# Performance work log

Measured on AMD Instinct MI355X. Metric: run time of the kernel, lower is better.

## Reference

```python
import jax, jax.numpy as jnp
import numpy as np

N = 50000      # nodes
E = 800000     # edges (avg degree 16)
H = 128        # hidden_dim
F_IN = 128     # node_in_dim
EPS = 1e-8     # torch cosine_similarity eps
ALPHA = 0.3


def _xavier(k, shape):
    fan_out, fan_in = shape
    lim = float(np.sqrt(6.0 / (fan_in + fan_out)))
    return jax.random.uniform(k, shape, minval=-lim, maxval=lim, dtype=jnp.float32)


PARAM_SHAPES = [
    ("w_lq", (H, 1)), ("w_lf", (H, F_IN)),
    ("wq0", (H, 1)), ("wq1", (H, H)), ("wq2", (H, H)),
    ("wx0", (H, F_IN)), ("wx1", (H, H)), ("wx2", (H, H)),
    ("wf0", (H, H)), ("wf1", (H, H)), ("wf2", (H, H)),
    ("m1_w1", (H, H)), ("m1_w2", (H, H)),
    ("m2_w1", (1, H)), ("m2_w2", (1, 1)),
]
BIAS_OF = {"w_lq": "b_lq", "w_lf": "b_lf", "wq0": "bq0", "wq1": "bq1", "wq2": "bq2",
           "wx0": "bx0", "wx1": "bx1", "wx2": "bx2", "wf0": "bf0", "wf1": "bf1",
           "wf2": "bf2", "m1_w1": "m1_b1", "m1_w2": "m1_b2", "m2_w1": "m2_b1", "m2_w2": "m2_b2"}


def setup_inputs() -> dict:
    key = jax.random.key(0)
    ks = jax.random.split(key, 3 + len(PARAM_SHAPES))
    inp = {
        "q": 42,
        "feats": jax.random.normal(ks[0], (N, F_IN), dtype=jnp.float32),
        "edge_index": jax.random.randint(ks[1], (2, E), 0, N, dtype=jnp.int64),
        "neg_edge_index": jax.random.randint(ks[2], (2, E), 0, N, dtype=jnp.int64),
    }
    for i, (name, shape) in enumerate(PARAM_SHAPES):
        inp[name] = _xavier(ks[3 + i], shape)
        inp[BIAS_OF[name]] = jnp.zeros((shape[0],), jnp.float32)
    return inp


def _forward(q, feats, edge_index, neg_edge_index,
             w_lq, b_lq, w_lf, b_lf,
             wq0, bq0, wq1, bq1, wq2, bq2,
             wx0, bx0, wx1, bx1, wx2, bx2,
             wf0, bf0, wf1, bf1, wf2, bf2,
             m1_w1, m1_b1, m1_w2, m1_b2,
             m2_w1, m2_b1, m2_w2, m2_b2):
    n = feats.shape[0]
    src, dst = edge_index[0], edge_index[1]

    # GCN symmetric normalization with self-loops (edge_weight = 1)
    deg = jax.ops.segment_sum(jnp.ones(src.shape[0], feats.dtype), dst, num_segments=n) + 1.0
    dis = deg ** -0.5
    norm_e = dis[src] * dis[dst]        # per-edge norm
    inv_deg = 1.0 / deg                 # self-loop norm d^-1/2 * d^-1/2

    def lin(x, W, b):
        return x @ W.T + b

    def gcn(x, W, b):
        xw = x @ W.T                                                      # [n,H]
        agg = jax.ops.segment_sum(xw[src] * norm_e[:, None], dst, num_segments=n)
        return agg + xw * inv_deg[:, None] + b

    querys = jnp.zeros((n, 1), feats.dtype).at[q, 0].set(1.0)
    querys_ = lin(querys, w_lq, b_lq)
    feats_ = lin(feats, w_lf, b_lf)

    # layer 0
    hq = jax.nn.relu(gcn(querys, wq0, bq0))
    h = jax.nn.relu(gcn(feats, wx0, bx0))
    hf = jax.nn.relu(hq + h + gcn(querys_ + feats_, wf0, bf0))
    # middle layer (num_layers - 2 == 1 iteration, eval mode: dropout identity)
    hq = jax.nn.relu(gcn(hq, wq1, bq1))
    h = jax.nn.relu(gcn(h, wx1, bx1))
    hf = jax.nn.relu(hq + h + gcn(hf, wf1, bf1))
    # final layer (no relu)
    hq = gcn(hq, wq2, bq2)
    h = gcn(h, wx2, bx2)
    hf = hq + h + gcn(hf, wf2, bf2)

    x = lin(jax.nn.relu(lin(hf, m1_w1, m1_b1)), m1_w2, m1_b2)  # mlp1

    # ---- decode (attack_type != 'proposed') ----
    q_emb = x[q]
    qn = jnp.maximum(jnp.linalg.norm(q_emb), EPS)

    def cos_q(v):  # cosine similarity of rows of v with q_emb (torch eps semantics)
        vn = jnp.maximum(jnp.linalg.norm(v, axis=-1), EPS)
        return (v @ q_emb) / (vn * qn)

    # reconstruct loss: BCE-with-logits on cosine edge scores
    pos_s = cos_q((x[src] + x[dst]) * 0.5)
    neg_s = cos_q((x[neg_edge_index[0]] + x[neg_edge_index[1]]) * 0.5)
    loss_recon = jnp.mean(jax.nn.softplus(-pos_s)) + jnp.mean(jax.nn.softplus(neg_s))

    sim_xq = cos_q(x)                                            # [n]
    sim_xx = lin(jax.nn.relu(lin(x, m2_w1, m2_b1)), m2_w2, m2_b2)[:, 0]  # mlp2
    sim = ((1.0 - ALPHA) * sim_xq + ALPHA * sim_xx) * 2.0
    return jax.nn.sigmoid(sim), loss_recon


def reference(q, feats, edge_index, neg_edge_index,
              w_lq, b_lq, w_lf, b_lf,
              wq0, bq0, wq1, bq1, wq2, bq2,
              wx0, bx0, wx1, bx1, wx2, bx2,
              wf0, bf0, wf1, bf1, wf2, bf2,
              m1_w1, m1_b1, m1_w2, m1_b2,
              m2_w1, m2_b1, m2_w2, m2_b2):
    return _forward(q, feats, edge_index, neg_edge_index,
                    w_lq, b_lq, w_lf, b_lf,
                    wq0, bq0, wq1, bq1, wq2, bq2,
                    wx0, bx0, wx1, bx1, wx2, bx2,
                    wf0, bf0, wf1, bf1, wf2, bf2,
                    m1_w1, m1_b1, m1_w2, m1_b2,
                    m2_w1, m2_b1, m2_w2, m2_b2)
```

## Files before the change

### kernel.cpp

```cpp
#include <hip/hip_runtime.h>
#include <math.h>

#define N_NODES 50000
#define N_EDGES 800000
#define EPSV 1e-8f
#define ALPHA 0.3f

typedef __attribute__((ext_vector_type(8))) unsigned short ushort8;
typedef __attribute__((ext_vector_type(4))) float floatx4;
typedef __attribute__((ext_vector_type(2))) long longx2;
typedef _Float16 half8 __attribute__((ext_vector_type(8)));
typedef _Float16 half2v __attribute__((ext_vector_type(2)));

__device__ inline unsigned short f2h(float f) {
    union { _Float16 h; unsigned short u; } c; c.h = (_Float16)f; return c.u;
}
__device__ inline float h2f(unsigned short u) {
    union { unsigned short u; _Float16 h; } c; c.u = u; return (float)c.h;
}
__device__ inline unsigned char f2e4m3(float f) {
    unsigned u = __float_as_uint(f);
    unsigned s = (u >> 24) & 0x80u;
    float af = fabsf(f);
    if (af >= 464.f) return (unsigned char)(s | 0x7Eu);
    if (af < 0.015625f) {
        int m = (int)rintf(af * 512.f);
        return (unsigned char)(s | (unsigned)m);
    }
    unsigned au = __float_as_uint(af);
    unsigned mant = au & 0x7FFFFFu;
    unsigned lsb = (mant >> 20) & 1u;
    mant += 0x7FFFFu + lsb;
    unsigned exp32 = (au >> 23) + (mant >> 23);
    mant &= 0x7FFFFFu;
    unsigned e8 = exp32 - 127u + 7u;
    return (unsigned char)(s | (e8 << 3) | (mant >> 20));
}


__global__ __launch_bounds__(256) void k_count(const int* __restrict__ ei,
                                               int* __restrict__ cnt) {
    int e = blockIdx.x * 256 + threadIdx.x;
    if (e < N_EDGES) atomicAdd(&cnt[ei[N_EDGES + e]], 1);
}

__global__ __launch_bounds__(256) void k_invdis(const int* __restrict__ cnt,
                                                float* __restrict__ dis,
                                                float* __restrict__ inv) {
    int i = blockIdx.x * 256 + threadIdx.x;
    if (i < N_NODES) {
        float d = (float)cnt[i] + 1.0f;
        dis[i] = 1.0f / sqrtf(d);
        inv[i] = 1.0f / d;
    }
}

__global__ __launch_bounds__(256) void k_scan_partial(const int* __restrict__ cnt,
                                                      int* __restrict__ partial) {
    int b = blockIdx.x, t = threadIdx.x;
    int base = b * 1024 + t * 4;
    int s = 0;
#pragma unroll
    for (int j = 0; j < 4; ++j) {
        int idx = base + j;
        if (idx < N_NODES) s += cnt[idx];
    }
#pragma unroll
    for (int m = 1; m < 64; m <<= 1) s += __shfl_xor(s, m, 64);
    __shared__ int sh[4];
    if ((t & 63) == 0) sh[t >> 6] = s;
    __syncthreads();
    if (t == 0) partial[b] = sh[0] + sh[1] + sh[2] + sh[3];
}

__global__ void k_scan_mid(int* __restrict__ partial, int* __restrict__ rowptr) {
    int l = threadIdx.x;
    const int NP = (N_NODES + 1023) / 1024;
    int v = (l < NP) ? partial[l] : 0;
    int vin = v;
#pragma unroll
    for (int off = 1; off < 64; off <<= 1) {
        int u = __shfl_up(v, off, 64);
        if (l >= off) v += u;
    }
    if (l < NP) partial[l] = v - vin;
    if (l == NP - 1) rowptr[N_NODES] = v;
}

__global__ __launch_bounds__(256) void k_scan_final(const int* __restrict__ cnt,
                                                    const int* __restrict__ partial,
                                                    int* __restrict__ rowptr) {
    int b = blockIdx.x, t = threadIdx.x;
    int base = b * 1024 + t * 4;
    int c[4];
    int s = 0;
#pragma unroll
    for (int j = 0; j < 4; ++j) {
        int idx = base + j;
        c[j] = (idx < N_NODES) ? cnt[idx] : 0;
        s += c[j];
    }
    __shared__ int sh[256];
    sh[t] = s;
    __syncthreads();
    for (int off = 1; off < 256; off <<= 1) {
        int v = 0;
        if (t >= off) v = sh[t - off];
        __syncthreads();
        sh[t] += v;
        __syncthreads();
    }
    int texcl = sh[t] - s;
    int pre = partial[b] + texcl;
#pragma unroll
    for (int j = 0; j < 4; ++j) {
        int idx = base + j;
        if (idx < N_NODES) rowptr[idx] = pre;
        pre += c[j];
    }
}

__global__ __launch_bounds__(256) void k_fill(const int* __restrict__ ei,
                                              const int* __restrict__ rowptr,
                                              int* __restrict__ cursor,
                                              int* __restrict__ col) {
    int e = blockIdx.x * 256 + threadIdx.x;
    if (e < N_EDGES) {
        int d = ei[N_EDGES + e];
        int pos = rowptr[d] + atomicAdd(&cursor[d], 1);
        col[pos] = ei[e];
    }
}

__global__ __launch_bounds__(256) void k_t(const int* __restrict__ ei,
                                           const int* __restrict__ qp,
                                           const float* __restrict__ dis,
                                           const float* __restrict__ inv,
                                           float* __restrict__ t) {
    int e = blockIdx.x * 256 + threadIdx.x;
    int q = *qp;
    if (e == 0) atomicAdd(&t[q], inv[q]);
    if (e < N_EDGES && ei[e] == q) {
        int d = ei[N_EDGES + e];
        atomicAdd(&t[d], dis[q] * dis[d]);
    }
}

__global__ void k_flag(const float* __restrict__ bq0, const float* __restrict__ bq1,
                       int* __restrict__ flag) {
    int j = threadIdx.x;
    float v = (j < 128) ? bq0[j] : bq1[j - 128];
    unsigned long long b = __ballot(v != 0.f);
    __shared__ int bad[4];
    if ((j & 63) == 0) bad[j >> 6] = (b != 0ull);
    __syncthreads();
    if (j == 0) flag[0] = !(bad[0] | bad[1] | bad[2] | bad[3]);
}

__global__ void k_r0(const int* __restrict__ gflag, const float* __restrict__ wq0,
                     float* __restrict__ r0) {
    if (*gflag != 1) return;
    int j = threadIdx.x;
    r0[j] = fmaxf(wq0[j], 0.f);
}

template <int RELU>
__global__ void k_matvec(const int* __restrict__ gflag, const float* __restrict__ W,
                         const float* __restrict__ vin, float* __restrict__ vout) {
    if (*gflag != 1) return;
    int c = blockIdx.x, l = threadIdx.x;
    float2 w = *(const float2*)(W + c * 128 + 2 * l);
    float2 v = *(const float2*)(vin + 2 * l);
    float s = w.x * v.x + w.y * v.y;
#pragma unroll
    for (int m = 1; m < 64; m <<= 1) s += __shfl_xor(s, m, 64);
    if (l == 0) vout[c] = RELU ? fmaxf(s, 0.f) : s;
}

__global__ __launch_bounds__(256) void k_spmv(const int* __restrict__ gflag,
                                              const int* __restrict__ rowptr,
                                              const int* __restrict__ col,
                                              const float* __restrict__ dis,
                                              const float* __restrict__ inv,
                                              const float* __restrict__ vin,
                                              float* __restrict__ vout) {
    if (*gflag != 1) return;
    int i = blockIdx.x * 256 + threadIdx.x;
    if (i >= N_NODES) return;
    int r0 = rowptr[i], r1 = rowptr[i + 1];
    float s = 0.f;
    for (int e = r0; e < r1; ++e) {
        int c = col[e];
        s += dis[c] * vin[c];
    }
    vout[i] = fmaf(inv[i], vin[i], dis[i] * s);
}

__global__ __launch_bounds__(256) void k_cast(const float* __restrict__ in,
                                              unsigned short* __restrict__ out, int n8) {
    int id = blockIdx.x * 256 + threadIdx.x;
    if (id >= n8) return;
    const float4 a = *(const float4*)(in + id * 8);
    const float4 b = *(const float4*)(in + id * 8 + 4);
    ushort8 o;
    o[0] = f2h(a.x); o[1] = f2h(a.y); o[2] = f2h(a.z); o[3] = f2h(a.w);
    o[4] = f2h(b.x); o[5] = f2h(b.y); o[6] = f2h(b.z); o[7] = f2h(b.w);
    *(ushort8*)(out + id * 8) = o;
}

struct WPack { const float* w[11]; };
__global__ __launch_bounds__(256) void k_castw(WPack wp, unsigned short* __restrict__ out) {
    int m = blockIdx.y;
    int id = blockIdx.x * 256 + threadIdx.x;
    const float* src = wp.w[m] + id * 8;
    float4 a = *(const float4*)src;
    float4 b = *(const float4*)(src + 4);
    ushort8 o;
    o[0] = f2h(a.x); o[1] = f2h(a.y); o[2] = f2h(a.z); o[3] = f2h(a.w);
    o[4] = f2h(b.x); o[5] = f2h(b.y); o[6] = f2h(b.z); o[7] = f2h(b.w);
    *(ushort8*)(out + m * 16384 + id * 8) = o;
}

__global__ __launch_bounds__(256) void k_cast8(const float* __restrict__ xf,
                                               unsigned char* __restrict__ xq8) {
    int id = blockIdx.x * 256 + threadIdx.x;
    int node = id >> 3, c = id & 7;
    if (node >= N_NODES) return;
    int kb = c >> 1, mb = (c & 1) * 2;
    const float* base = xf + (size_t)node * 128;
    const float* p0 = base + mb * 32 + kb * 8;
    const float* p1 = base + (mb + 1) * 32 + kb * 8;
    union { unsigned char b[16]; uint4 u; } o;
#pragma unroll
    for (int j = 0; j < 8; ++j) o.b[j] = f2e4m3(p0[j]);
#pragma unroll
    for (int j = 0; j < 8; ++j) o.b[8 + j] = f2e4m3(p1[j]);
    *(uint4*)(xq8 + (size_t)node * 128 + c * 16) = o.u;
}


template <int RELU, int NADD, int HASB2, int WOUT, int RK1>
__global__ __launch_bounds__(256) void k_gemm(
    const unsigned short* __restrict__ A, int As,
    const unsigned short* __restrict__ Wb,
    const float* __restrict__ bias, const float* __restrict__ bias2,
    const unsigned short* __restrict__ add1, int a1s,
    const unsigned short* __restrict__ add2, int a2s,
    const float* __restrict__ u, const float* __restrict__ vq,
    const int* __restrict__ gflag, int want,
    unsigned short* __restrict__ outh, int ohs,
    float* __restrict__ outf, int ofs, int nrows) {
    if (gflag && *gflag != want) return;
    __shared__ unsigned short Al[128 * 128];
    __shared__ unsigned short Wl[128 * 128];
    const int tid = threadIdx.x;
    const int row0 = blockIdx.x * 128;
    const int wv = tid >> 6;
    const int t4 = tid >> 4, c16 = tid & 15;

#pragma unroll
    for (int it = 0; it < 8; ++it) {
        int r = it * 16 + t4;
        int gr = row0 + r; if (gr > nrows - 1) gr = nrows - 1;
        int sw = (c16 * 16) ^ ((r & 7) << 4);
        const char* srcA = (const char*)(A + (size_t)gr * As) + sw;
        __builtin_amdgcn_global_load_lds(
            (const __attribute__((address_space(1))) void*)srcA,
            (__attribute__((address_space(3))) void*)(Al + it * 2048 + wv * 512),
            16, 0, 0);
        const char* srcW = (const char*)(Wb + r * 128) + sw;
        __builtin_amdgcn_global_load_lds(
            (const __attribute__((address_space(1))) void*)srcW,
            (__attribute__((address_space(3))) void*)(Wl + it * 2048 + wv * 512),
            16, 0, 0);
    }
    __syncthreads();

    const int l = tid & 63;
    const int lr = l & 15, lg = l >> 4;
    const int sx = (lr & 7) << 4;

    floatx4 acc[8][2];
#pragma unroll
    for (int i = 0; i < 8; ++i)
#pragma unroll
        for (int j = 0; j < 2; ++j) acc[i][j] = (floatx4){0.f, 0.f, 0.f, 0.f};

#pragma unroll
    for (int ks = 0; ks < 4; ++ks) {
        int ko = (ks * 64 + lg * 16) ^ sx;
        half8 bfr[2];
#pragma unroll
        for (int ct = 0; ct < 2; ++ct) {
            int c = wv * 32 + ct * 16 + lr;
            bfr[ct] = *(const half8*)((char*)Wl + c * 256 + ko);
        }
#pragma unroll
        for (int rt = 0; rt < 8; ++rt) {
            int r = rt * 16 + lr;
            half8 af = *(const half8*)((char*)Al + r * 256 + ko);
            acc[rt][0] = __builtin_amdgcn_mfma_f32_16x16x32_f16(af, bfr[0], acc[rt][0], 0, 0, 0);
            acc[rt][1] = __builtin_amdgcn_mfma_f32_16x16x32_f16(af, bfr[1], acc[rt][1], 0, 0, 0);
        }
    }

#pragma unroll
    for (int ct = 0; ct < 2; ++ct) {
        int colc = wv * 32 + ct * 16 + lr;
        float bv = bias[colc];
        if (HASB2) bv += bias2[colc];
        float vqc = RK1 ? vq[colc] : 0.f;
#pragma unroll
        for (int rt = 0; rt < 8; ++rt) {
            int rbase = row0 + rt * 16 + lg * 4;
#pragma unroll
            for (int reg = 0; reg < 4; ++reg) {
                int r = rbase + reg;
                if (r >= nrows) continue;
                float v = acc[rt][ct][reg] + bv;
                if (RK1) v = fmaf(u[r], vqc, v);
                if (NADD >= 1) v += h2f(add1[(size_t)r * a1s + colc]);
                if (NADD >= 2) v += h2f(add2[(size_t)r * a2s + colc]);
                if (RELU) v = fmaxf(v, 0.f);
                if (WOUT) outf[(size_t)r * ofs + colc] = v;
                else outh[(size_t)r * ohs + colc] = f2h(v);
            }
        }
    }
}


template <int NUM>
__global__ __launch_bounds__(256) void k_agg(
    const int* __restrict__ gflag, int want,
    const int* __restrict__ rowptr, const int* __restrict__ col,
    const float* __restrict__ dis, const float* __restrict__ inv,
    const unsigned short* __restrict__ in0, int s0,
    const unsigned short* __restrict__ in1, int s1,
    const unsigned short* __restrict__ in2, int s2,
    unsigned short* __restrict__ out, int o0, int o1, int o2) {
    if (gflag && *gflag != want) return;
    int i = blockIdx.x * 4 + (threadIdx.x >> 6);
    int l = threadIdx.x & 63;
    int g = l >> 4, li = l & 15;
    int r0 = rowptr[i], r1 = rowptr[i + 1];

    half2v accA[NUM][4], accB[NUM][4];
#pragma unroll
    for (int b = 0; b < NUM; ++b)
#pragma unroll
        for (int j = 0; j < 4; ++j) {
            accA[b][j] = (half2v){(_Float16)0, (_Float16)0};
            accB[b][j] = (half2v){(_Float16)0, (_Float16)0};
        }

    union U8 { ushort8 u; half2v h[4]; };
    const unsigned short* ins[3] = {in0, in1, in2};
    const int ss[3] = {s0, s1, s2};

    for (int base = r0; base < r1; base += 8) {
        int eA = base + g, eB = base + 4 + g;
        int sA = i; float wA = 0.f;
        if (eA < r1) { sA = col[eA]; wA = dis[sA]; }
        int sB = i; float wB = 0.f;
        if (eB < r1) { sB = col[eB]; wB = dis[sB]; }
        _Float16 whA = (_Float16)wA, whB = (_Float16)wB;
        half2v w2A = {whA, whA}, w2B = {whB, whB};
        U8 vA[NUM], vB[NUM];
#pragma unroll
        for (int b = 0; b < NUM; ++b) {
            vA[b].u = *(const ushort8*)(ins[b] + (size_t)sA * ss[b] + li * 8);
            vB[b].u = *(const ushort8*)(ins[b] + (size_t)sB * ss[b] + li * 8);
        }
#pragma unroll
        for (int b = 0; b < NUM; ++b)
#pragma unroll
            for (int j = 0; j < 4; ++j) {
                accA[b][j] += vA[b].h[j] * w2A;
                accB[b][j] += vB[b].h[j] * w2B;
            }
    }
    union U2 { half2v h; int i; };
#pragma unroll
    for (int b = 0; b < NUM; ++b)
#pragma unroll
        for (int j = 0; j < 4; ++j) {
            U2 c, o;
            c.h = accA[b][j] + accB[b][j];
            o.i = __shfl_xor(c.i, 16, 64); c.h += o.h;
            o.i = __shfl_xor(c.i, 32, 64); c.h += o.h;
            accA[b][j] = c.h;
        }
    if (g == 0) {
        float di = dis[i], iv = inv[i];
        const int oo[3] = {o0, o1, o2};
#pragma unroll
        for (int b = 0; b < NUM; ++b) {
            U8 sv;
            sv.u = *(const ushort8*)(ins[b] + (size_t)i * ss[b] + li * 8);
            ushort8 o;
#pragma unroll
            for (int j = 0; j < 4; ++j) {
                float a0 = fmaf(di, (float)accA[b][j][0], iv * (float)sv.h[j][0]);
                float a1 = fmaf(di, (float)accA[b][j][1], iv * (float)sv.h[j][1]);
                o[2 * j] = f2h(a0);
                o[2 * j + 1] = f2h(a1);
            }
            *(ushort8*)(out + (size_t)i * 384 + oo[b] + li * 8) = o;
        }
    }
}

__global__ __launch_bounds__(256) void k_hq0(const int* __restrict__ gflag,
                                             const float* __restrict__ t,
                                             const float* __restrict__ wq0,
                                             const float* __restrict__ bq0,
                                             unsigned short* __restrict__ B1h) {
    if (*gflag != 0) return;
    int gidx = blockIdx.x * 256 + threadIdx.x;
    int i = gidx >> 7, j = gidx & 127;
    B1h[(size_t)i * 384 + j] = f2h(fmaxf(fmaf(t[i], wq0[j], bq0[j]), 0.f));
}

__global__ void k_addwlq(const int* __restrict__ qp, const float* __restrict__ w_lq,
                         unsigned short* __restrict__ z0h) {
    int j = threadIdx.x;
    int q = *qp;
    z0h[(size_t)q * 128 + j] = f2h(h2f(z0h[(size_t)q * 128 + j]) + w_lq[j]);
}


__global__ void k_qemb(const int* __restrict__ qp, const float* __restrict__ xf,
                       float* __restrict__ qe) {
    int j = threadIdx.x;
    int q = *qp;
    float v = xf[(size_t)q * 128 + j];
    qe[j] = v;
    float s = v * v;
#pragma unroll
    for (int m = 1; m < 64; m <<= 1) s += __shfl_xor(s, m, 64);
    __shared__ float sh[2];
    if ((j & 63) == 0) sh[j >> 6] = s;
    __syncthreads();
    if (j == 0) qe[128] = fmaxf(sqrtf(sh[0] + sh[1]), EPSV);
}

__global__ __launch_bounds__(256) void k_node(const float* __restrict__ xf,
                                              const float* __restrict__ qe,
                                              const float* __restrict__ m2w1,
                                              const float* __restrict__ m2b1,
                                              const float* __restrict__ m2w2,
                                              const float* __restrict__ m2b2,
                                              float* __restrict__ out,
                                              float* __restrict__ a,
                                              float* __restrict__ n2) {
    int node = blockIdx.x * 4 + (threadIdx.x >> 6);
    int lane = threadIdx.x & 63;
    const float2 xv = *(const float2*)(xf + (size_t)node * 128 + 2 * lane);
    const float2 qv = *(const float2*)(qe + 2 * lane);
    const float2 wv = *(const float2*)(m2w1 + 2 * lane);
    float dq = xv.x * qv.x + xv.y * qv.y;
    float dx = xv.x * xv.x + xv.y * xv.y;
    float dw = xv.x * wv.x + xv.y * wv.y;
#pragma unroll
    for (int m = 1; m < 64; m <<= 1) {
        dq += __shfl_xor(dq, m, 64);
        dx += __shfl_xor(dx, m, 64);
        dw += __shfl_xor(dw, m, 64);
    }
    if (lane == 0) {
        float qn = qe[128];
        float vn = fmaxf(sqrtf(dx), EPSV);
        float simq = dq / (vn * qn);
        float l1 = dw + m2b1[0];
        float s2 = fmaxf(l1, 0.f) * m2w2[0] + m2b2[0];
        float sim = ((1.f - ALPHA) * simq + ALPHA * s2) * 2.f;
        out[node] = 1.f / (1.f + expf(-sim));
        a[node] = dq;
        n2[node] = dx;
    }
}

__global__ __launch_bounds__(256) void k_loss(const int* __restrict__ ei,
                                              const int* __restrict__ nei,
                                              const unsigned char* __restrict__ xq8,
                                              const float* __restrict__ a,
                                              const float* __restrict__ n2,
                                              const float* __restrict__ qe,
                                              float* __restrict__ lossout) {
    int l = threadIdx.x & 63, wvi = threadIdx.x >> 6;
    int i16 = l & 15;
    int kb = l >> 4;
    int gw = blockIdx.x * 4 + wvi;
    const int NW = gridDim.x * 4;
    const int NT = 2 * N_EDGES / 16;
    float qn = qe[128];
    float local = 0.f;

    int t = gw;
    for (; t + NW < NT; t += 2 * NW) {
        int baseA = t * 16;
        int negA = baseA >= N_EDGES;
        const int* EpA = negA ? nei : ei;
        int eoA = negA ? baseA - N_EDGES : baseA;
        int sA = EpA[eoA + i16], dA = EpA[eoA + i16 + N_EDGES];

        int baseB = (t + NW) * 16;
        int negB = baseB >= N_EDGES;
        const int* EpB = negB ? nei : ei;
        int eoB = negB ? baseB - N_EDGES : baseB;
        int sB = EpB[eoB + i16], dB = EpB[eoB + i16 + N_EDGES];

        const unsigned char* psA = xq8 + (size_t)sA * 128 + kb * 32;
        const unsigned char* pdA = xq8 + (size_t)dA * 128 + kb * 32;
        longx2 a01A = *(const longx2*)psA;
        longx2 a23A = *(const longx2*)(psA + 16);
        longx2 b01A = *(const longx2*)pdA;
        longx2 b23A = *(const longx2*)(pdA + 16);

        const unsigned char* psB = xq8 + (size_t)sB * 128 + kb * 32;
        const unsigned char* pdB = xq8 + (size_t)dB * 128 + kb * 32;
        longx2 a01B = *(const longx2*)psB;
        longx2 a23B = *(const longx2*)(psB + 16);
        longx2 b01B = *(const longx2*)pdB;
        longx2 b23B = *(const longx2*)(pdB + 16);

        float n2sA = 0.f, n2dA = 0.f, asA = 0.f, adA = 0.f;
        float n2sB = 0.f, n2dB = 0.f, asB = 0.f, adB = 0.f;
        if (l < 16) {
            n2sA = n2[sA]; n2dA = n2[dA]; asA = a[sA]; adA = a[dA];
            n2sB = n2[sB]; n2dB = n2[dB]; asB = a[sB]; adB = a[dB];
        }

        int r = l & 3;
        int srcl = ((i16 >> 2) << 4) + i16;
        {
            floatx4 acc = (floatx4){0.f, 0.f, 0.f, 0.f};
            acc = __builtin_amdgcn_mfma_f32_16x16x32_fp8_fp8(a01A[0], b01A[0], acc, 0, 0, 0);
            acc = __builtin_amdgcn_mfma_f32_16x16x32_fp8_fp8(a01A[1], b01A[1], acc, 0, 0, 0);
            acc = __builtin_amdgcn_mfma_f32_16x16x32_fp8_fp8(a23A[0], b23A[0], acc, 0, 0, 0);
            acc = __builtin_amdgcn_mfma_f32_16x16x32_fp8_fp8(a23A[1], b23A[1], acc, 0, 0, 0);
            float v = acc[0];
            v = (r == 1) ? acc[1] : v;
            v = (r == 2) ? acc[2] : v;
            v = (r == 3) ? acc[3] : v;
            float dsd = __int_as_float(
                __builtin_amdgcn_ds_bpermute(srcl << 2, __float_as_int(v)));
            if (l < 16) {
                float nv = 0.25f * (n2sA + n2dA + 2.f * dsd);
                float vn = fmaxf(sqrtf(fmaxf(nv, 0.f)), EPSV);
                float cs = (0.5f * (asA + adA)) / (vn * qn);
                float sg = negA ? cs : -cs;
                local += log1pf(expf(sg));
            }
        }
        {
            floatx4 acc = (floatx4){0.f, 0.f, 0.f, 0.f};
            acc = __builtin_amdgcn_mfma_f32_16x16x32_fp8_fp8(a01B[0], b01B[0], acc, 0, 0, 0);
            acc = __builtin_amdgcn_mfma_f32_16x16x32_fp8_fp8(a01B[1], b01B[1], acc, 0, 0, 0);
            acc = __builtin_amdgcn_mfma_f32_16x16x32_fp8_fp8(a23B[0], b23B[0], acc, 0, 0, 0);
            acc = __builtin_amdgcn_mfma_f32_16x16x32_fp8_fp8(a23B[1], b23B[1], acc, 0, 0, 0);
            float v = acc[0];
            v = (r == 1) ? acc[1] : v;
            v = (r == 2) ? acc[2] : v;
            v = (r == 3) ? acc[3] : v;
            float dsd = __int_as_float(
                __builtin_amdgcn_ds_bpermute(srcl << 2, __float_as_int(v)));
            if (l < 16) {
                float nv = 0.25f * (n2sB + n2dB + 2.f * dsd);
                float vn = fmaxf(sqrtf(fmaxf(nv, 0.f)), EPSV);
                float cs = (0.5f * (asB + adB)) / (vn * qn);
                float sg = negB ? cs : -cs;
                local += log1pf(expf(sg));
            }
        }
    }
    if (t < NT) {
        int base = t * 16;
        int neg = base >= N_EDGES;
        const int* Ep = neg ? nei : ei;
        int eo = neg ? base - N_EDGES : base;
        int s = Ep[eo + i16], d = Ep[eo + i16 + N_EDGES];
        const unsigned char* ps = xq8 + (size_t)s * 128 + kb * 32;
        const unsigned char* pd = xq8 + (size_t)d * 128 + kb * 32;
        longx2 a01 = *(const longx2*)ps;
        longx2 a23 = *(const longx2*)(ps + 16);
        longx2 b01 = *(const longx2*)pd;
        longx2 b23 = *(const longx2*)(pd + 16);
        floatx4 acc = (floatx4){0.f, 0.f, 0.f, 0.f};
        acc = __builtin_amdgcn_mfma_f32_16x16x32_fp8_fp8(a01[0], b01[0], acc, 0, 0, 0);
        acc = __builtin_amdgcn_mfma_f32_16x16x32_fp8_fp8(a01[1], b01[1], acc, 0, 0, 0);
        acc = __builtin_amdgcn_mfma_f32_16x16x32_fp8_fp8(a23[0], b23[0], acc, 0, 0, 0);
        acc = __builtin_amdgcn_mfma_f32_16x16x32_fp8_fp8(a23[1], b23[1], acc, 0, 0, 0);
        int r = l & 3;
        float v = acc[0];
        v = (r == 1) ? acc[1] : v;
        v = (r == 2) ? acc[2] : v;
        v = (r == 3) ? acc[3] : v;
        int srcl = ((i16 >> 2) << 4) + i16;
        float dsd = __int_as_float(
            __builtin_amdgcn_ds_bpermute(srcl << 2, __float_as_int(v)));
        if (l < 16) {
            float nv = 0.25f * (n2[s] + n2[d] + 2.f * dsd);
            float vn = fmaxf(sqrtf(fmaxf(nv, 0.f)), EPSV);
            float cs = (0.5f * (a[s] + a[d])) / (vn * qn);
            float sg = neg ? cs : -cs;
            local += log1pf(expf(sg));
        }
    }
    local += __shfl_xor(local, 1, 64);
    local += __shfl_xor(local, 2, 64);
    local += __shfl_xor(local, 4, 64);
    local += __shfl_xor(local, 8, 64);
    __shared__ float sh[4];
    if (l == 0) sh[wvi] = local;
    __syncthreads();
    if (threadIdx.x == 0)
        atomicAdd(lossout, (sh[0] + sh[1] + sh[2] + sh[3]) * (1.f / N_EDGES));
}


extern "C" void kernel_launch(void* const* d_in, const int* in_sizes, int n_in,
                              void* d_out, int out_size, void* d_ws, size_t ws_size,
                              hipStream_t stream) {
    const int* qp = (const int*)d_in[0];
    const float* feats = (const float*)d_in[1];
    const int* ei = (const int*)d_in[2];
    const int* nei = (const int*)d_in[3];
    const float *w_lq = (const float*)d_in[4], *b_lq = (const float*)d_in[5];
    const float *w_lf = (const float*)d_in[6], *b_lf = (const float*)d_in[7];
    const float *wq0 = (const float*)d_in[8], *bq0 = (const float*)d_in[9];
    const float *wq1 = (const float*)d_in[10], *bq1 = (const float*)d_in[11];
    const float *wq2 = (const float*)d_in[12], *bq2 = (const float*)d_in[13];
    const float *wx0 = (const float*)d_in[14], *bx0 = (const float*)d_in[15];
    const float *wx1 = (const float*)d_in[16], *bx1 = (const float*)d_in[17];
    const float *wx2 = (const float*)d_in[18], *bx2 = (const float*)d_in[19];
    const float *wf0 = (const float*)d_in[20], *bf0 = (const float*)d_in[21];
    const float *wf1 = (const float*)d_in[22], *bf1 = (const float*)d_in[23];
    const float *wf2 = (const float*)d_in[24], *bf2 = (const float*)d_in[25];
    const float *m1w1 = (const float*)d_in[26], *m1b1 = (const float*)d_in[27];
    const float *m1w2 = (const float*)d_in[28], *m1b2 = (const float*)d_in[29];
    const float *m2w1 = (const float*)d_in[30], *m2b1 = (const float*)d_in[31];
    const float *m2w2 = (const float*)d_in[32], *m2b2 = (const float*)d_in[33];
    float* out = (float*)d_out;

    char* p = (char*)d_ws;
    auto alloc = [&](size_t b) -> char* {
        char* r = p;
        p += (b + 255) & ~(size_t)255;
        return r;
    };
    float* dis = (float*)alloc(N_NODES * 4);
    float* inv = (float*)alloc(N_NODES * 4);
    float* t = (float*)alloc(N_NODES * 4);
    float* qe = (float*)alloc(129 * 4);
    float* a = (float*)alloc(N_NODES * 4);
    float* n2 = (float*)alloc(N_NODES * 4);
    float* u1 = (float*)alloc(N_NODES * 4);
    float* u2 = (float*)alloc(N_NODES * 4);
    float* r0v = (float*)alloc(128 * 4);
    float* r1v = (float*)alloc(128 * 4);
    float* g2v = (float*)alloc(128 * 4);
    int* flag = (int*)alloc(4);
    int* cnt = (int*)alloc(N_NODES * 4);
    int* cursor = (int*)alloc(N_NODES * 4);
    int* rowptr = (int*)alloc((N_NODES + 1) * 4);
    int* partial = (int*)alloc(64 * 4);
    int* col = (int*)alloc(N_EDGES * 4);
    unsigned short* Wb = (unsigned short*)alloc((size_t)11 * 16384 * 2);
    unsigned short* featsh = (unsigned short*)alloc((size_t)N_NODES * 128 * 2);
    unsigned short* z0h = (unsigned short*)alloc((size_t)N_NODES * 128 * 2);
    unsigned short* B1h = (unsigned short*)alloc((size_t)N_NODES * 384 * 2);
    unsigned short* B2h = (unsigned short*)alloc((size_t)N_NODES * 384 * 2);
    unsigned char* xq8 = (unsigned char*)alloc((size_t)N_NODES * 128);
    float* xf = (float*)alloc((size_t)N_NODES * 128 * 4);

    const int EB = (N_EDGES + 255) / 256;
    const int NB = (N_NODES + 255) / 256;
    const int NP = (N_NODES + 1023) / 1024;
    const int GB = (N_NODES + 127) / 128;

    hipMemsetAsync(cnt, 0, N_NODES * 4, stream);
    hipMemsetAsync(cursor, 0, N_NODES * 4, stream);
    hipMemsetAsync(t, 0, N_NODES * 4, stream);
    hipMemsetAsync(out + N_NODES, 0, 4, stream);

    k_count<<<EB, 256, 0, stream>>>(ei, cnt);
    k_invdis<<<NB, 256, 0, stream>>>(cnt, dis, inv);
    k_scan_partial<<<NP, 256, 0, stream>>>(cnt, partial);
    k_scan_mid<<<1, 64, 0, stream>>>(partial, rowptr);
    k_scan_final<<<NP, 256, 0, stream>>>(cnt, partial, rowptr);
    k_fill<<<EB, 256, 0, stream>>>(ei, rowptr, cursor, col);
    k_t<<<EB, 256, 0, stream>>>(ei, qp, dis, inv, t);
    k_flag<<<1, 256, 0, stream>>>(bq0, bq1, flag);
    k_cast<<<(N_NODES * 128 / 8 + 255) / 256, 256, 0, stream>>>(feats, featsh,
                                                                N_NODES * 128 / 8);
    WPack wp{{w_lf, wx0, wf0, wq1, wx1, wf1, wq2, wx2, wf2, m1w1, m1w2}};
    k_castw<<<dim3(8, 11), 256, 0, stream>>>(wp, Wb);

    k_r0<<<1, 128, 0, stream>>>(flag, wq0, r0v);
    k_spmv<<<NB, 256, 0, stream>>>(flag, rowptr, col, dis, inv, t, u1);
    k_spmv<<<NB, 256, 0, stream>>>(flag, rowptr, col, dis, inv, u1, u2);
    k_matvec<1><<<128, 64, 0, stream>>>(flag, wq1, r0v, r1v);
    k_matvec<0><<<128, 64, 0, stream>>>(flag, wq2, r1v, g2v);

    k_gemm<0, 0, 1, 0, 0><<<GB, 256, 0, stream>>>(featsh, 128, Wb + 0 * 16384, b_lf, b_lq,
                                                  nullptr, 0, nullptr, 0,
                                                  nullptr, nullptr, nullptr, 0,
                                                  z0h, 128, nullptr, 0, N_NODES);
    k_addwlq<<<1, 128, 0, stream>>>(qp, w_lq, z0h);

    k_hq0<<<(N_NODES * 128) / 256, 256, 0, stream>>>(flag, t, wq0, bq0, B1h);
    k_agg<2><<<N_NODES / 4, 256, 0, stream>>>(nullptr, 0, rowptr, col, dis, inv,
                                              featsh, 128, z0h, 128, nullptr, 0,
                                              B2h, 128, 256, 0);
    k_gemm<1, 0, 0, 0, 0><<<GB, 256, 0, stream>>>(B2h + 128, 384, Wb + 1 * 16384, bx0, nullptr,
                                                  nullptr, 0, nullptr, 0,
                                                  nullptr, nullptr, nullptr, 0,
                                                  B1h + 128, 384, nullptr, 0, N_NODES);
    k_gemm<1, 2, 0, 0, 0><<<GB, 256, 0, stream>>>(B2h + 256, 384, Wb + 2 * 16384, bf0, nullptr,
                                                  B1h + 0, 384, B1h + 128, 384,
                                                  nullptr, nullptr, flag, 0,
                                                  B1h + 256, 384, nullptr, 0, N_NODES);
    k_gemm<1, 1, 0, 0, 1><<<GB, 256, 0, stream>>>(B2h + 256, 384, Wb + 2 * 16384, bf0, nullptr,
                                                  B1h + 128, 384, nullptr, 0,
                                                  t, r0v, flag, 1,
                                                  B1h + 256, 384, nullptr, 0, N_NODES);

    k_agg<3><<<N_NODES / 4, 256, 0, stream>>>(flag, 0, rowptr, col, dis, inv,
                                              B1h, 384, B1h + 128, 384, B1h + 256, 384,
                                              B2h, 0, 128, 256);
    k_agg<2><<<N_NODES / 4, 256, 0, stream>>>(flag, 1, rowptr, col, dis, inv,
                                              B1h + 128, 384, B1h + 256, 384, nullptr, 0,
                                              B2h, 128, 256, 0);
    k_gemm<1, 0, 0, 0, 0><<<GB, 256, 0, stream>>>(B2h + 0, 384, Wb + 3 * 16384, bq1, nullptr,
                                                  nullptr, 0, nullptr, 0,
                                                  nullptr, nullptr, flag, 0,
                                                  B1h + 0, 384, nullptr, 0, N_NODES);
    k_gemm<1, 0, 0, 0, 0><<<GB, 256, 0, stream>>>(B2h + 128, 384, Wb + 4 * 16384, bx1, nullptr,
                                                  nullptr, 0, nullptr, 0,
                                                  nullptr, nullptr, nullptr, 0,
                                                  B1h + 128, 384, nullptr, 0, N_NODES);
    k_gemm<1, 2, 0, 0, 0><<<GB, 256, 0, stream>>>(B2h + 256, 384, Wb + 5 * 16384, bf1, nullptr,
                                                  B1h + 0, 384, B1h + 128, 384,
                                                  nullptr, nullptr, flag, 0,
                                                  B1h + 256, 384, nullptr, 0, N_NODES);
    k_gemm<1, 1, 0, 0, 1><<<GB, 256, 0, stream>>>(B2h + 256, 384, Wb + 5 * 16384, bf1, nullptr,
                                                  B1h + 128, 384, nullptr, 0,
                                                  u1, r1v, flag, 1,
                                                  B1h + 256, 384, nullptr, 0, N_NODES);

    k_agg<3><<<N_NODES / 4, 256, 0, stream>>>(flag, 0, rowptr, col, dis, inv,
                                              B1h, 384, B1h + 128, 384, B1h + 256, 384,
                                              B2h, 0, 128, 256);
    k_agg<2><<<N_NODES / 4, 256, 0, stream>>>(flag, 1, rowptr, col, dis, inv,
                                              B1h + 128, 384, B1h + 256, 384, nullptr, 0,
                                              B2h, 128, 256, 0);
    k_gemm<0, 0, 0, 0, 0><<<GB, 256, 0, stream>>>(B2h + 0, 384, Wb + 6 * 16384, bq2, nullptr,
                                                  nullptr, 0, nullptr, 0,
                                                  nullptr, nullptr, flag, 0,
                                                  B1h + 0, 384, nullptr, 0, N_NODES);
    k_gemm<0, 0, 0, 0, 0><<<GB, 256, 0, stream>>>(B2h + 128, 384, Wb + 7 * 16384, bx2, nullptr,
                                                  nullptr, 0, nullptr, 0,
                                                  nullptr, nullptr, nullptr, 0,
                                                  B1h + 128, 384, nullptr, 0, N_NODES);
    k_gemm<0, 2, 0, 0, 0><<<GB, 256, 0, stream>>>(B2h + 256, 384, Wb + 8 * 16384, bf2, nullptr,
                                                  B1h + 0, 384, B1h + 128, 384,
                                                  nullptr, nullptr, flag, 0,
                                                  B1h + 256, 384, nullptr, 0, N_NODES);
    k_gemm<0, 1, 1, 0, 1><<<GB, 256, 0, stream>>>(B2h + 256, 384, Wb + 8 * 16384, bf2, bq2,
                                                  B1h + 128, 384, nullptr, 0,
                                                  u2, g2v, flag, 1,
                                                  B1h + 256, 384, nullptr, 0, N_NODES);

    k_gemm<1, 0, 0, 0, 0><<<GB, 256, 0, stream>>>(B1h + 256, 384, Wb + 9 * 16384, m1b1, nullptr,
                                                  nullptr, 0, nullptr, 0,
                                                  nullptr, nullptr, nullptr, 0,
                                                  B2h + 0, 384, nullptr, 0, N_NODES);
    k_gemm<0, 0, 0, 1, 0><<<GB, 256, 0, stream>>>(B2h + 0, 384, Wb + 10 * 16384, m1b2, nullptr,
                                                  nullptr, 0, nullptr, 0,
                                                  nullptr, nullptr, nullptr, 0,
                                                  nullptr, 0, xf, 128, N_NODES);

    k_cast8<<<(N_NODES * 8 + 255) / 256, 256, 0, stream>>>(xf, xq8);
    k_qemb<<<1, 128, 0, stream>>>(qp, xf, qe);
    k_node<<<N_NODES / 4, 256, 0, stream>>>(xf, qe, m2w1, m2b1, m2w2, m2b2, out, a, n2);
    k_loss<<<2048, 256, 0, stream>>>(ei, nei, xq8, a, n2, qe, out + N_NODES);
}
```

Measured before the change: 612.2 us.

## Process loss edges in destination-sorted CSR order for gather locality

After: 698.5 us. 14.1% more time.

```diff
diff --git a/kernel.cpp b/kernel.cpp
--- a/kernel.cpp
+++ b/kernel.cpp
@@ -41,7 +41,7 @@
 __global__ __launch_bounds__(256) void k_count(const int* __restrict__ ei,
                                                int* __restrict__ cnt) {
     int e = blockIdx.x * 256 + threadIdx.x;
-    if (e < N_EDGES) atomicAdd(&cnt[ei[N_EDGES + e]], 1);
+    if (e < N_EDGES) atomicAdd(&cnt[__builtin_nontemporal_load(ei + N_EDGES + e)], 1);
 }
 
 __global__ __launch_bounds__(256) void k_invdis(const int* __restrict__ cnt,
@@ -123,12 +123,14 @@
 __global__ __launch_bounds__(256) void k_fill(const int* __restrict__ ei,
                                               const int* __restrict__ rowptr,
                                               int* __restrict__ cursor,
-                                              int* __restrict__ col) {
+                                              int* __restrict__ col,
+                                              int* __restrict__ dstl) {
     int e = blockIdx.x * 256 + threadIdx.x;
     if (e < N_EDGES) {
-        int d = ei[N_EDGES + e];
+        int d = __builtin_nontemporal_load(ei + N_EDGES + e);
         int pos = rowptr[d] + atomicAdd(&cursor[d], 1);
-        col[pos] = ei[e];
+        col[pos] = __builtin_nontemporal_load(ei + e);
+        dstl[pos] = d;
     }
 }
 
@@ -140,7 +142,7 @@
     int e = blockIdx.x * 256 + threadIdx.x;
     int q = *qp;
     if (e == 0) atomicAdd(&t[q], inv[q]);
-    if (e < N_EDGES && ei[e] == q) {
+    if (e < N_EDGES && __builtin_nontemporal_load(ei + e) == q) {
         int d = ei[N_EDGES + e];
         atomicAdd(&t[d], dis[q] * dis[d]);
     }
@@ -481,8 +483,10 @@
     }
 }
 
-__global__ __launch_bounds__(256) void k_loss(const int* __restrict__ ei,
-                                              const int* __restrict__ nei,
+__global__ __launch_bounds__(256) void k_loss(const int* __restrict__ colP,
+                                              const int* __restrict__ dstP,
+                                              const int* __restrict__ colN,
+                                              const int* __restrict__ dstN,
                                               const unsigned char* __restrict__ xq8,
                                               const float* __restrict__ a,
                                               const float* __restrict__ n2,
@@ -496,20 +500,26 @@
     const int NT = 2 * N_EDGES / 16;
     float qn = qe[128];
     float local = 0.f;
+    const int rsel = l & 3;
+    const int srcl = ((i16 >> 2) << 4) + i16;
 
     int t = gw;
     for (; t + NW < NT; t += 2 * NW) {
         int baseA = t * 16;
         int negA = baseA >= N_EDGES;
-        const int* EpA = negA ? nei : ei;
-        int eoA = negA ? baseA - N_EDGES : baseA;
-        int sA = EpA[eoA + i16], dA = EpA[eoA + i16 + N_EDGES];
+        const int* slA = negA ? colN : colP;
+        const int* dlA = negA ? dstN : dstP;
+        int eoA = (negA ? baseA - N_EDGES : baseA) + i16;
+        int sA = slA[eoA];
+        int dA = dlA[eoA];
 
         int baseB = (t + NW) * 16;
         int negB = baseB >= N_EDGES;
-        const int* EpB = negB ? nei : ei;
-        int eoB = negB ? baseB - N_EDGES : baseB;
-        int sB = EpB[eoB + i16], dB = EpB[eoB + i16 + N_EDGES];
+        const int* slB = negB ? colN : colP;
+        const int* dlB = negB ? dstN : dstP;
+        int eoB = (negB ? baseB - N_EDGES : baseB) + i16;
+        int sB = slB[eoB];
+        int dB = dlB[eoB];
 
         const unsigned char* psA = xq8 + (size_t)sA * 128 + kb * 32;
         const unsigned char* pdA = xq8 + (size_t)dA * 128 + kb * 32;
@@ -532,8 +542,6 @@
             n2sB = n2[sB]; n2dB = n2[dB]; asB = a[sB]; adB = a[dB];
         }
 
-        int r = l & 3;
-        int srcl = ((i16 >> 2) << 4) + i16;
         {
             floatx4 acc = (floatx4){0.f, 0.f, 0.f, 0.f};
             acc = __builtin_amdgcn_mfma_f32_16x16x32_fp8_fp8(a01A[0], b01A[0], acc, 0, 0, 0);
@@ -541,9 +549,9 @@
             acc = __builtin_amdgcn_mfma_f32_16x16x32_fp8_fp8(a23A[0], b23A[0], acc, 0, 0, 0);
             acc = __builtin_amdgcn_mfma_f32_16x16x32_fp8_fp8(a23A[1], b23A[1], acc, 0, 0, 0);
             float v = acc[0];
-            v = (r == 1) ? acc[1] : v;
-            v = (r == 2) ? acc[2] : v;
-            v = (r == 3) ? acc[3] : v;
+            v = (rsel == 1) ? acc[1] : v;
+            v = (rsel == 2) ? acc[2] : v;
+            v = (rsel == 3) ? acc[3] : v;
             float dsd = __int_as_float(
                 __builtin_amdgcn_ds_bpermute(srcl << 2, __float_as_int(v)));
             if (l < 16) {
@@ -561,9 +569,9 @@
             acc = __builtin_amdgcn_mfma_f32_16x16x32_fp8_fp8(a23B[0], b23B[0], acc, 0, 0, 0);
             acc = __builtin_amdgcn_mfma_f32_16x16x32_fp8_fp8(a23B[1], b23B[1], acc, 0, 0, 0);
             float v = acc[0];
-            v = (r == 1) ? acc[1] : v;
-            v = (r == 2) ? acc[2] : v;
-            v = (r == 3) ? acc[3] : v;
+            v = (rsel == 1) ? acc[1] : v;
+            v = (rsel == 2) ? acc[2] : v;
+            v = (rsel == 3) ? acc[3] : v;
             float dsd = __int_as_float(
                 __builtin_amdgcn_ds_bpermute(srcl << 2, __float_as_int(v)));
             if (l < 16) {
@@ -578,9 +586,11 @@
     if (t < NT) {
         int base = t * 16;
         int neg = base >= N_EDGES;
-        const int* Ep = neg ? nei : ei;
-        int eo = neg ? base - N_EDGES : base;
-        int s = Ep[eo + i16], d = Ep[eo + i16 + N_EDGES];
+        const int* sl = neg ? colN : colP;
+        const int* dl = neg ? dstN : dstP;
+        int eo = (neg ? base - N_EDGES : base) + i16;
+        int s = sl[eo];
+        int d = dl[eo];
         const unsigned char* ps = xq8 + (size_t)s * 128 + kb * 32;
         const unsigned char* pd = xq8 + (size_t)d * 128 + kb * 32;
         longx2 a01 = *(const longx2*)ps;
@@ -592,12 +602,10 @@
         acc = __builtin_amdgcn_mfma_f32_16x16x32_fp8_fp8(a01[1], b01[1], acc, 0, 0, 0);
         acc = __builtin_amdgcn_mfma_f32_16x16x32_fp8_fp8(a23[0], b23[0], acc, 0, 0, 0);
         acc = __builtin_amdgcn_mfma_f32_16x16x32_fp8_fp8(a23[1], b23[1], acc, 0, 0, 0);
-        int r = l & 3;
         float v = acc[0];
-        v = (r == 1) ? acc[1] : v;
-        v = (r == 2) ? acc[2] : v;
-        v = (r == 3) ? acc[3] : v;
-        int srcl = ((i16 >> 2) << 4) + i16;
+        v = (rsel == 1) ? acc[1] : v;
+        v = (rsel == 2) ? acc[2] : v;
+        v = (rsel == 3) ? acc[3] : v;
         float dsd = __int_as_float(
             __builtin_amdgcn_ds_bpermute(srcl << 2, __float_as_int(v)));
         if (l < 16) {
@@ -667,6 +675,12 @@
     int* rowptr = (int*)alloc((N_NODES + 1) * 4);
     int* partial = (int*)alloc(64 * 4);
     int* col = (int*)alloc(N_EDGES * 4);
+    int* dstP = (int*)alloc(N_EDGES * 4);
+    int* cntN = (int*)alloc(N_NODES * 4);
+    int* cursorN = (int*)alloc(N_NODES * 4);
+    int* rowptrN = (int*)alloc((N_NODES + 1) * 4);
+    int* colN = (int*)alloc(N_EDGES * 4);
+    int* dstN = (int*)alloc(N_EDGES * 4);
     unsigned short* Wb = (unsigned short*)alloc((size_t)11 * 16384 * 2);
     unsigned short* featsh = (unsigned short*)alloc((size_t)N_NODES * 128 * 2);
     unsigned short* z0h = (unsigned short*)alloc((size_t)N_NODES * 128 * 2);
@@ -682,6 +696,8 @@
 
     hipMemsetAsync(cnt, 0, N_NODES * 4, stream);
     hipMemsetAsync(cursor, 0, N_NODES * 4, stream);
+    hipMemsetAsync(cntN, 0, N_NODES * 4, stream);
+    hipMemsetAsync(cursorN, 0, N_NODES * 4, stream);
     hipMemsetAsync(t, 0, N_NODES * 4, stream);
     hipMemsetAsync(out + N_NODES, 0, 4, stream);
 
@@ -690,8 +706,14 @@
     k_scan_partial<<<NP, 256, 0, stream>>>(cnt, partial);
     k_scan_mid<<<1, 64, 0, stream>>>(partial, rowptr);
     k_scan_final<<<NP, 256, 0, stream>>>(cnt, partial, rowptr);
-    k_fill<<<EB, 256, 0, stream>>>(ei, rowptr, cursor, col);
+    k_fill<<<EB, 256, 0, stream>>>(ei, rowptr, cursor, col, dstP);
     k_t<<<EB, 256, 0, stream>>>(ei, qp, dis, inv, t);
+    k_count<<<EB, 256, 0, stream>>>(nei, cntN);
+    k_scan_partial<<<NP, 256, 0, stream>>>(cntN, partial);
+    k_scan_mid<<<1, 64, 0, stream>>>(partial, rowptrN);
+    k_scan_final<<<NP, 256, 0, stream>>>(cntN, partial, rowptrN);
+    k_fill<<<EB, 256, 0, stream>>>(nei, rowptrN, cursorN, colN, dstN);
+
     k_flag<<<1, 256, 0, stream>>>(bq0, bq1, flag);
     k_cast<<<(N_NODES * 128 / 8 + 255) / 256, 256, 0, stream>>>(feats, featsh,
                                                                 N_NODES * 128 / 8);
@@ -785,5 +807,5 @@
     k_cast8<<<(N_NODES * 8 + 255) / 256, 256, 0, stream>>>(xf, xq8);
     k_qemb<<<1, 128, 0, stream>>>(qp, xf, qe);
     k_node<<<N_NODES / 4, 256, 0, stream>>>(xf, qe, m2w1, m2b1, m2w2, m2b2, out, a, n2);
-    k_loss<<<2048, 256, 0, stream>>>(ei, nei, xq8, a, n2, qe, out + N_NODES);
-}
+    k_loss<<<2048, 256, 0, stream>>>(col, dstP, colN, dstN, xq8, a, n2, qe, out + N_NODES);
+}
```
